# Optimization experiments

Measured on AMD Instinct MI355X. Metric: run time of the kernel, lower is better.

The kernel has to match this reference:

```python
import jax, jax.numpy as jnp
import numpy as np

N_QKV = 64
N_EMBED = 2048
B = 4
T = 2048  # must equal N_EMBED because the module's causal mask is n_embed x n_embed


def setup_inputs() -> dict:
    key = jax.random.key(0)
    ks = jax.random.split(key, 7)
    s = 1.0 / np.sqrt(N_EMBED)
    return {
        "x": jax.random.normal(ks[0], (B, T, N_EMBED), dtype=jnp.float32),
        "Wq": jax.random.normal(ks[1], (N_QKV, N_EMBED), dtype=jnp.float32) * s,
        "bq": jnp.zeros((N_QKV,), dtype=jnp.float32),
        "Wk": jax.random.normal(ks[2], (N_QKV, N_EMBED), dtype=jnp.float32) * s,
        "bk": jnp.zeros((N_QKV,), dtype=jnp.float32),
        "Wv": jax.random.normal(ks[3], (N_QKV, N_EMBED), dtype=jnp.float32) * s,
        "bv": jnp.zeros((N_QKV,), dtype=jnp.float32),
    }


def reference(x, Wq, bq, Wk, bk, Wv, bv):
    # Linear projections: torch nn.Linear computes x @ W.T + b
    q = jnp.einsum("bte,qe->btq", x, Wq) + bq  # [B, T, n_qkv]
    k = jnp.einsum("bte,qe->btq", x, Wk) + bk
    v = jnp.einsum("bte,qe->btq", x, Wv) + bv
    scale = 1.0 / jnp.sqrt(jnp.asarray(N_QKV, dtype=x.dtype))
    logits = jnp.einsum("btq,bsq->bts", q, k) * scale  # [B, T, T]
    # causal mask: upper triangle (strictly above diagonal) -> -inf
    causal = jnp.tril(jnp.ones((T, T), dtype=bool))
    logits = jnp.where(causal, logits, jnp.asarray(-jnp.inf, dtype=logits.dtype))
    probs = jax.nn.softmax(logits, axis=-1)
    return jnp.einsum("bts,bsq->btq", probs, v)  # [B, T, n_qkv]
```

## Files before the change

kernel.cpp:

```cpp
#include <hip/hip_runtime.h>
#include <hip/hip_bf16.h>

#define T_SEQ 2048
#define E_DIM 2048
#define D_HEAD 64
#define B_SZ 4
#define NROWS (B_SZ * T_SEQ)

typedef __attribute__((ext_vector_type(8))) short bf16x8;
typedef __attribute__((ext_vector_type(4))) float f32x4;
typedef __attribute__((ext_vector_type(4))) unsigned short u16x4;
typedef __attribute__((ext_vector_type(8))) unsigned short u16x8;

__device__ __forceinline__ unsigned short f2bf(float x) {
    __hip_bfloat16 h = __float2bfloat16(x);
    return *reinterpret_cast<unsigned short*>(&h);
}

__device__ __forceinline__ u16x8 cvt8(float4 a, float4 b) {
    u16x8 t;
    t[0] = f2bf(a.x); t[1] = f2bf(a.y); t[2] = f2bf(a.z); t[3] = f2bf(a.w);
    t[4] = f2bf(b.x); t[5] = f2bf(b.y); t[6] = f2bf(b.z); t[7] = f2bf(b.w);
    return t;
}

__device__ __forceinline__ u16x4 cvt4(float4 a) {
    u16x4 t;
    t[0] = f2bf(a.x); t[1] = f2bf(a.y); t[2] = f2bf(a.z); t[3] = f2bf(a.w);
    return t;
}

__device__ __forceinline__ bf16x8 ldfrag(const unsigned short* p) {
    u16x4 lo = *(const u16x4*)p;
    u16x4 hi = *(const u16x4*)(p + 16);
    bf16x8 f;
    #pragma unroll
    for (int j = 0; j < 4; ++j) { f[j] = (short)lo[j]; f[4 + j] = (short)hi[j]; }
    return f;
}

__global__ __launch_bounds__(256) void wcvt_kernel(
    const float* __restrict__ Wq, const float* __restrict__ Wk,
    const float* __restrict__ Wv, unsigned short* __restrict__ Wp)
{
    const int gid = blockIdx.x * 256 + threadIdx.x;
    const int l    = gid & 63;
    const int k32  = (gid >> 6) & 63;
    const int f    = gid >> 12;
    const int r    = l & 15;
    const int g    = l >> 4;
    const int n    = 16 * f + r;
    const int pj   = n >> 6;
    const int o    = n & 63;
    const float* __restrict__ src = (pj == 0) ? Wq : (pj == 1) ? Wk : Wv;
    const float* p = src + (size_t)o * E_DIM + k32 * 32 + g * 4;
    float4 a = *(const float4*)p;
    float4 b = *(const float4*)(p + 16);
    *(u16x8*)(Wp + (size_t)gid * 8) = cvt8(a, b);
}

__global__ __launch_bounds__(768) void proj_mfma_kernel(
    const float* __restrict__ x, const unsigned short* __restrict__ Wp,
    const float* __restrict__ bq, const float* __restrict__ bk,
    const float* __restrict__ bv,
    __hip_bfloat16* __restrict__ qb, __hip_bfloat16* __restrict__ kb,
    __hip_bfloat16* __restrict__ vb)
{
    __shared__ unsigned short xs[2][32 * 72];

    const int tid  = threadIdx.x;
    const int w    = tid >> 6;
    const int l    = tid & 63;
    const int r    = l & 15;
    const int g    = l >> 4;
    const int wm   = (w >= 6) ? 1 : 0;
    const int wf   = (w >= 6) ? (w - 6) : w;
    const int row0 = blockIdx.x * 32;

    const bool stager = tid < 512;
    const int srow = tid >> 4;
    const int sc4  = (tid & 15) * 4;
    const float* xptr = x + (size_t)(row0 + srow) * E_DIM + sc4;

    const unsigned short* wb = Wp + (size_t)l * 8;

    f32x4 acc[2];
    acc[0] = (f32x4){0.f, 0.f, 0.f, 0.f};
    acc[1] = (f32x4){0.f, 0.f, 0.f, 0.f};

    float4 x0, xw, xf1;
    if (stager) {
        x0  = *(const float4*)(xptr);
        xw  = *(const float4*)(xptr + 64);
        xf1 = *(const float4*)(xptr + 128);
    }
    bf16x8 bcur[2][2];
    #pragma unroll
    for (int kk = 0; kk < 2; ++kk)
        #pragma unroll
        for (int ff = 0; ff < 2; ++ff)
            bcur[kk][ff] = *(const bf16x8*)(wb + (size_t)((2 * wf + ff) * 64 + kk) * 512);
    if (stager) *(u16x4*)&xs[0][srow * 72 + sc4] = cvt4(x0);
    __syncthreads();

    for (int t = 0; t < 32; ++t) {
        const int cur = t & 1;

        float4 xf0;
        if (t < 29 && stager) xf0 = *(const float4*)(xptr + (t + 3) * 64);
        bf16x8 bnx[2][2];
        if (t < 31) {
            #pragma unroll
            for (int kk = 0; kk < 2; ++kk)
                #pragma unroll
                for (int ff = 0; ff < 2; ++ff)
                    bnx[kk][ff] = *(const bf16x8*)(
                        wb + (size_t)((2 * wf + ff) * 64 + 2 * (t + 1) + kk) * 512);
        }

        bf16x8 af[2];
        #pragma unroll
        for (int kk = 0; kk < 2; ++kk)
            af[kk] = ldfrag(&xs[cur][(wm * 16 + r) * 72 + kk * 32 + 4 * g]);

        if (t < 31 && stager) *(u16x4*)&xs[cur ^ 1][srow * 72 + sc4] = cvt4(xw);

        #pragma unroll
        for (int kk = 0; kk < 2; ++kk)
            #pragma unroll
            for (int ff = 0; ff < 2; ++ff)
                acc[ff] = __builtin_amdgcn_mfma_f32_16x16x32_bf16(
                    af[kk], bcur[kk][ff], acc[ff], 0, 0, 0);

        __syncthreads();

        xw = xf1; xf1 = xf0;
        #pragma unroll
        for (int kk = 0; kk < 2; ++kk)
            #pragma unroll
            for (int ff = 0; ff < 2; ++ff)
                bcur[kk][ff] = bnx[kk][ff];
    }

    #pragma unroll
    for (int ff = 0; ff < 2; ++ff) {
        const int f  = 2 * wf + ff;
        const int n  = 16 * f + r;
        const int pj = n >> 6;
        const int o  = n & 63;
        const float* bias = (pj == 0) ? bq : (pj == 1) ? bk : bv;
        __hip_bfloat16* dst = (pj == 0) ? qb : (pj == 1) ? kb : vb;
        const float scale = (pj == 0) ? 0.18033688011112042f : 1.0f;
        const float bv_ = bias[o];
        #pragma unroll
        for (int j = 0; j < 4; ++j) {
            const int row = row0 + wm * 16 + 4 * g + j;
            dst[(size_t)row * D_HEAD + o] =
                __float2bfloat16((acc[ff][j] + bv_) * scale);
        }
    }
}

#define LDK 72
#define LDV 68
#define LDP 68

__global__ __launch_bounds__(128) void attn_part_kernel(
    const __hip_bfloat16* __restrict__ qg, const __hip_bfloat16* __restrict__ kg,
    const __hip_bfloat16* __restrict__ vg, float* __restrict__ Op,
    float* __restrict__ Ml, int tpc, int nch)
{
    const int qt = blockIdx.x;
    const int ch = blockIdx.y;
    const int total64 = qt / 2 + 1;
    if (ch * tpc >= total64) return;

    __shared__ unsigned short Kl[64 * LDK];
    __shared__ unsigned short Vt[64 * LDV];
    __shared__ unsigned short Pl[2 * 16 * LDP];

    const int tid = threadIdx.x;
    const int w   = tid >> 6;
    const int l   = tid & 63;
    const int r   = l & 15;
    const int g   = l >> 4;
    const int q0  = qt * 32;
    const int b   = blockIdx.z;
    const size_t base = (size_t)b * T_SEQ;

    const unsigned short* qb16 = (const unsigned short*)qg;
    const unsigned short* kb16 = (const unsigned short*)kg;
    const unsigned short* vb16 = (const unsigned short*)vg;

    const unsigned short* qrow = qb16 + (base + q0 + 16 * w + r) * D_HEAD;
    bf16x8 qf[2];
    #pragma unroll
    for (int kk = 0; kk < 2; ++kk)
        qf[kk] = ldfrag(qrow + 32 * kk + 4 * g);

    f32x4 acc_o[4];
    #pragma unroll
    for (int dn = 0; dn < 4; ++dn) acc_o[dn] = (f32x4){0.f, 0.f, 0.f, 0.f};
    float m4[4] = {-1e30f, -1e30f, -1e30f, -1e30f};
    float l4[4] = {0.f, 0.f, 0.f, 0.f};

    unsigned short* pw = &Pl[w * 16 * LDP];
    const int ntiles = min(tpc, total64 - ch * tpc);
    const int y = tid & 15, z = tid >> 4;

    for (int it = 0; it < ntiles; ++it) {
        const int s0 = (ch * tpc + it) * 64;

        __syncthreads();
        for (int c = tid; c < 512; c += 128) {
            const int row = c >> 3;
            const int dc  = (c & 7) * 8;
            *(u16x8*)(&Kl[row * LDK + dc]) =
                *(const u16x8*)(kb16 + (base + s0 + row) * D_HEAD + dc);
        }
        #pragma unroll
        for (int m = 0; m < 4; ++m) {
            const int sl = 2 * (z + 8 * m);
            const int d0 = y * 4;
            u16x4 va = *(const u16x4*)(vb16 + (base + s0 + sl) * D_HEAD + d0);
            u16x4 vb2 = *(const u16x4*)(vb16 + (base + s0 + sl + 1) * D_HEAD + d0);
            #pragma unroll
            for (int i = 0; i < 4; ++i) {
                unsigned int pr = (unsigned int)(unsigned short)va[i] |
                                  ((unsigned int)(unsigned short)vb2[i] << 16);
                *(unsigned int*)&Vt[(d0 + i) * LDV + sl] = pr;
            }
        }
        __syncthreads();

        f32x4 s_acc[4];
        #pragma unroll
        for (int nt = 0; nt < 4; ++nt) s_acc[nt] = (f32x4){0.f, 0.f, 0.f, 0.f};
        #pragma unroll
        for (int nt = 0; nt < 4; ++nt)
            #pragma unroll
            for (int kk = 0; kk < 2; ++kk) {
                bf16x8 bf = ldfrag(&Kl[(nt * 16 + r) * LDK + kk * 32 + 4 * g]);
                s_acc[nt] = __builtin_amdgcn_mfma_f32_16x16x32_bf16(qf[kk], bf, s_acc[nt], 0, 0, 0);
            }

        if (s0 + 64 > q0) {
            #pragma unroll
            for (int nt = 0; nt < 4; ++nt)
                #pragma unroll
                for (int j = 0; j < 4; ++j)
                    if (s0 + nt * 16 + r > q0 + 16 * w + 4 * g + j)
                        s_acc[nt][j] = -1e30f;
        }

        float tm[4];
        #pragma unroll
        for (int j = 0; j < 4; ++j)
            tm[j] = fmaxf(fmaxf(s_acc[0][j], s_acc[1][j]),
                          fmaxf(s_acc[2][j], s_acc[3][j]));
        #pragma unroll
        for (int mask = 1; mask < 16; mask <<= 1)
            #pragma unroll
            for (int j = 0; j < 4; ++j)
                tm[j] = fmaxf(tm[j], __shfl_xor(tm[j], mask));

        float p[4][4], rs[4];
        #pragma unroll
        for (int j = 0; j < 4; ++j) {
            const float mn = fmaxf(m4[j], tm[j]);
            const float sc = exp2f(m4[j] - mn);
            m4[j] = mn;
            rs[j] = 0.f;
            #pragma unroll
            for (int nt = 0; nt < 4; ++nt) {
                p[nt][j] = exp2f(s_acc[nt][j] - mn);
                rs[j] += p[nt][j];
            }
            l4[j] *= sc;
            acc_o[0][j] *= sc; acc_o[1][j] *= sc;
            acc_o[2][j] *= sc; acc_o[3][j] *= sc;
        }
        #pragma unroll
        for (int mask = 1; mask < 16; mask <<= 1)
            #pragma unroll
            for (int j = 0; j < 4; ++j)
                rs[j] += __shfl_xor(rs[j], mask);
        #pragma unroll
        for (int j = 0; j < 4; ++j) l4[j] += rs[j];

        #pragma unroll
        for (int nt = 0; nt < 4; ++nt)
            #pragma unroll
            for (int j = 0; j < 4; ++j)
                pw[(4 * g + j) * LDP + nt * 16 + r] = f2bf(p[nt][j]);

        bf16x8 pf[2];
        #pragma unroll
        for (int kk = 0; kk < 2; ++kk)
            pf[kk] = ldfrag(&pw[r * LDP + kk * 32 + 4 * g]);

        #pragma unroll
        for (int dn = 0; dn < 4; ++dn)
            #pragma unroll
            for (int kk = 0; kk < 2; ++kk) {
                bf16x8 vf = ldfrag(&Vt[(dn * 16 + r) * LDV + kk * 32 + 4 * g]);
                acc_o[dn] = __builtin_amdgcn_mfma_f32_16x16x32_bf16(pf[kk], vf, acc_o[dn], 0, 0, 0);
            }
    }

    const size_t pidx = ((size_t)(b * 64 + qt) * nch + ch);
    float* op = Op + pidx * 2048;
    #pragma unroll
    for (int j = 0; j < 4; ++j) {
        const int row = 16 * w + 4 * g + j;
        #pragma unroll
        for (int dn = 0; dn < 4; ++dn)
            op[row * 64 + dn * 16 + r] = acc_o[dn][j];
        if (r == 0) {
            Ml[pidx * 64 + row]      = m4[j];
            Ml[pidx * 64 + 32 + row] = l4[j];
        }
    }
}

__global__ __launch_bounds__(256) void attn_combine_kernel(
    const float* __restrict__ Op, const float* __restrict__ Ml,
    float* __restrict__ out, int tpc, int nch)
{
    const int qt = blockIdx.x;
    const int b  = blockIdx.y;
    const int total64 = qt / 2 + 1;
    const int nact = (total64 + tpc - 1) / tpc;
    const size_t pbase = (size_t)(b * 64 + qt) * nch;

    __shared__ float wgt[8][32];
    __shared__ float linv[32];

    const int tid = threadIdx.x;
    if (tid < 32) {
        float M = -1e30f;
        for (int c = 0; c < nact; ++c)
            M = fmaxf(M, Ml[(pbase + c) * 64 + tid]);
        float L = 0.f;
        for (int c = 0; c < nact; ++c) {
            float wv = exp2f(Ml[(pbase + c) * 64 + tid] - M);
            wgt[c][tid] = wv;
            L += wv * Ml[(pbase + c) * 64 + 32 + tid];
        }
        linv[tid] = 1.0f / L;
    }
    __syncthreads();

    const int d  = tid & 63;
    const int r0 = tid >> 6;
    for (int row = r0; row < 32; row += 4) {
        float a = 0.f;
        for (int c = 0; c < nact; ++c)
            a += wgt[c][row] * Op[(pbase + c) * 2048 + row * 64 + d];
        out[((size_t)b * T_SEQ + qt * 32 + row) * D_HEAD + d] = a * linv[row];
    }
}

extern "C" void kernel_launch(void* const* d_in, const int* in_sizes, int n_in,
                              void* d_out, int out_size, void* d_ws, size_t ws_size,
                              hipStream_t stream) {
    const float* x  = (const float*)d_in[0];
    const float* Wq = (const float*)d_in[1];
    const float* bq = (const float*)d_in[2];
    const float* Wk = (const float*)d_in[3];
    const float* bk = (const float*)d_in[4];
    const float* Wv = (const float*)d_in[5];
    const float* bv = (const float*)d_in[6];
    float* out = (float*)d_out;

    __hip_bfloat16* qb = (__hip_bfloat16*)d_ws;
    __hip_bfloat16* kb = qb + (size_t)NROWS * D_HEAD;
    __hip_bfloat16* vb = kb + (size_t)NROWS * D_HEAD;
    unsigned short* Wp = (unsigned short*)(vb + (size_t)NROWS * D_HEAD);
    float* Op = (float*)((char*)d_ws + (4u << 20));

    int nch = 8;
    while (nch > 1 &&
           (4u << 20) + (size_t)256 * nch * (2048 + 64) * 4 > ws_size)
        nch >>= 1;
    const int tpc = 32 / nch;
    float* Ml = Op + (size_t)256 * nch * 2048;

    wcvt_kernel<<<192, 256, 0, stream>>>(Wq, Wk, Wv, Wp);
    proj_mfma_kernel<<<NROWS / 32, 768, 0, stream>>>(x, Wp, bq, bk, bv, qb, kb, vb);
    attn_part_kernel<<<dim3(64, nch, B_SZ), 128, 0, stream>>>(qb, kb, vb, Op, Ml, tpc, nch);
    attn_combine_kernel<<<dim3(64, B_SZ), 256, 0, stream>>>(Op, Ml, out, tpc, nch);
}
```

Baseline: 73.21 us.

## Prefetch next K/V tile into registers and use LDS-only barriers

The attention loop now issues global loads for the next K/V tile into registers right after the LDS-store barrier, so they overlap with the current tile's QK, softmax and PV compute. Only LDS stores happen at the top of each iteration. __syncthreads is replaced by an lgkmcnt-only wait plus s_barrier, so barriers no longer wait on outstanding global loads (vmcnt). This costs extra registers for the staged data, which may reduce occupancy. It also relies on the barrier-without-fence ordering being correct.

```diff
diff --git a/kernel.cpp b/kernel.cpp
--- a/kernel.cpp
+++ b/kernel.cpp
@@ -37,6 +37,11 @@
     #pragma unroll
     for (int j = 0; j < 4; ++j) { f[j] = (short)lo[j]; f[4 + j] = (short)hi[j]; }
     return f;
+}
+
+__device__ __forceinline__ void lds_fence_barrier() {
+    asm volatile("s_waitcnt lgkmcnt(0)" ::: "memory");
+    __builtin_amdgcn_s_barrier();
 }
 
 __global__ __launch_bounds__(256) void wcvt_kernel(
@@ -101,7 +106,7 @@
         for (int ff = 0; ff < 2; ++ff)
             bcur[kk][ff] = *(const bf16x8*)(wb + (size_t)((2 * wf + ff) * 64 + kk) * 512);
     if (stager) *(u16x4*)&xs[0][srow * 72 + sc4] = cvt4(x0);
-    __syncthreads();
+    lds_fence_barrier();
 
     for (int t = 0; t < 32; ++t) {
         const int cur = t & 1;
@@ -132,7 +137,7 @@
                 acc[ff] = __builtin_amdgcn_mfma_f32_16x16x32_bf16(
                     af[kk], bcur[kk][ff], acc[ff], 0, 0, 0);
 
-        __syncthreads();
+        lds_fence_barrier();
 
         xw = xf1; xf1 = xf0;
         #pragma unroll
@@ -207,31 +212,52 @@
     unsigned short* pw = &Pl[w * 16 * LDP];
     const int ntiles = min(tpc, total64 - ch * tpc);
     const int y = tid & 15, z = tid >> 4;
-
-    for (int it = 0; it < ntiles; ++it) {
-        const int s0 = (ch * tpc + it) * 64;
-
-        __syncthreads();
-        for (int c = tid; c < 512; c += 128) {
-            const int row = c >> 3;
-            const int dc  = (c & 7) * 8;
-            *(u16x8*)(&Kl[row * LDK + dc]) =
-                *(const u16x8*)(kb16 + (base + s0 + row) * D_HEAD + dc);
+    const int s0base = ch * tpc * 64;
+
+    u16x8 kr[4];
+    u16x4 va4[4], vb4[4];
+
+    auto issue = [&](int s0) {
+        #pragma unroll
+        for (int i = 0; i < 4; ++i) {
+            const int c = tid + i * 128;
+            kr[i] = *(const u16x8*)(kb16 + (base + s0 + (c >> 3)) * D_HEAD + (c & 7) * 8);
         }
         #pragma unroll
         for (int m = 0; m < 4; ++m) {
             const int sl = 2 * (z + 8 * m);
             const int d0 = y * 4;
-            u16x4 va = *(const u16x4*)(vb16 + (base + s0 + sl) * D_HEAD + d0);
-            u16x4 vb2 = *(const u16x4*)(vb16 + (base + s0 + sl + 1) * D_HEAD + d0);
+            va4[m] = *(const u16x4*)(vb16 + (base + s0 + sl) * D_HEAD + d0);
+            vb4[m] = *(const u16x4*)(vb16 + (base + s0 + sl + 1) * D_HEAD + d0);
+        }
+    };
+
+    issue(s0base);
+
+    for (int it = 0; it < ntiles; ++it) {
+        const int s0 = s0base + it * 64;
+
+        __builtin_amdgcn_s_barrier();
+
+        #pragma unroll
+        for (int i = 0; i < 4; ++i) {
+            const int c = tid + i * 128;
+            *(u16x8*)(&Kl[(c >> 3) * LDK + (c & 7) * 8]) = kr[i];
+        }
+        #pragma unroll
+        for (int m = 0; m < 4; ++m) {
+            const int sl = 2 * (z + 8 * m);
+            const int d0 = y * 4;
             #pragma unroll
             for (int i = 0; i < 4; ++i) {
-                unsigned int pr = (unsigned int)(unsigned short)va[i] |
-                                  ((unsigned int)(unsigned short)vb2[i] << 16);
+                unsigned int pr = (unsigned int)(unsigned short)va4[m][i] |
+                                  ((unsigned int)(unsigned short)vb4[m][i] << 16);
                 *(unsigned int*)&Vt[(d0 + i) * LDV + sl] = pr;
             }
         }
-        __syncthreads();
+        lds_fence_barrier();
+
+        if (it + 1 < ntiles) issue(s0 + 64);
 
         f32x4 s_acc[4];
         #pragma unroll
```

Result: faster. 69.79 us (-4.7%).
